# Performance work log

Measured on AMD Instinct MI355X. Metric: run time of the kernel, lower is better.

## Reference

```python
import jax, jax.numpy as jnp
import numpy as np

V, H, T, B = 32000, 1024, 512, 64

def setup_inputs() -> dict:
    key = jax.random.key(0)
    ks = jax.random.split(key, 20)
    tokens = jax.random.randint(ks[0], (T, B), 0, V)
    s_emb = 1.0 / np.sqrt(V)
    s_g = 1.0 / np.sqrt(2 * H)
    d = {
        'tokens': tokens,
        'emb_w': jax.random.uniform(ks[1], (H, V), jnp.float32, -s_emb, s_emb),
        'emb_b': jax.random.uniform(ks[2], (H,), jnp.float32, -s_emb, s_emb),
    }
    i = 3
    for pfx in ('fwd', 'bwd'):
        for g in ('i', 'o', 'f', 'g'):
            d[f'{pfx}_w{g}'] = jax.random.uniform(ks[i], (H, 2 * H), jnp.float32, -s_g, s_g); i += 1
            d[f'{pfx}_b{g}'] = jax.random.uniform(ks[i % 20], (H,), jnp.float32, -s_g, s_g)
    return d

def _run_lstm(xs, wi, bi, wo, bo, wf, bf, wg, bg):
    # xs: [T, B, H]; manual LSTM recurrence via lax.scan
    h0 = jnp.zeros((xs.shape[1], H), xs.dtype)
    c0 = jnp.zeros((xs.shape[1], H), xs.dtype)
    def step(carry, x):
        h, c = carry
        comb = jnp.concatenate([x, h], axis=1)          # [B, 2H]
        ig = jax.nn.sigmoid(comb @ wi.T + bi)
        og = jax.nn.sigmoid(comb @ wo.T + bo)
        fg = jax.nn.sigmoid(comb @ wf.T + bf)
        cg = jnp.tanh(comb @ wg.T + bg)
        c = fg * c + ig * cg
        h = og * jnp.tanh(c)
        return (h, c), (h, c)
    _, (hs, cs) = jax.lax.scan(step, (h0, c0), xs)
    return hs, cs                                       # [T, B, H] each

def reference(tokens, emb_w, emb_b,
              fwd_wi, fwd_bi, fwd_wo, fwd_bo, fwd_wf, fwd_bf, fwd_wg, fwd_bg,
              bwd_wi, bwd_bi, bwd_wo, bwd_bo, bwd_wf, bwd_bf, bwd_wg, bwd_bg):
    # one_hot(tokens) @ emb_w.T + emb_b == emb_w.T[tokens] + emb_b (dropout in eval mode)
    emb = emb_w.T[tokens] + emb_b                        # [T, B, H]
    f_hs, f_cs = _run_lstm(emb, fwd_wi, fwd_bi, fwd_wo, fwd_bo, fwd_wf, fwd_bf, fwd_wg, fwd_bg)
    # backward pass over reversed sequence; outputs kept in reversed-scan order,
    # matching the original's un-realigned list concatenation.
    b_hs, b_cs = _run_lstm(emb[::-1], bwd_wi, bwd_bi, bwd_wo, bwd_bo, bwd_wf, bwd_bf, bwd_wg, bwd_bg)
    hidden_states = jnp.concatenate([f_hs, b_hs], axis=2)   # [T, B, 2H]
    cell_states = jnp.concatenate([f_cs, b_cs], axis=2)     # [T, B, 2H]
    return hidden_states, cell_states
```

## Files before the change

### kernel.cpp

```cpp
#include <hip/hip_runtime.h>
#include <cstdint>
#include <cstddef>

#define V_SZ 32000
#define H_SZ 1024
#define T_SZ 512
#define B_SZ 64

typedef short short8 __attribute__((ext_vector_type(8)));
typedef float f32x4 __attribute__((ext_vector_type(4)));
typedef unsigned long long u64;

__device__ __forceinline__ short f2bf(float f) {
  union { float f; unsigned u; } v; v.f = f;
  unsigned r = (v.u + 0x7fffu + ((v.u >> 16) & 1u)) >> 16;
  return (short)r;
}

__device__ __forceinline__ unsigned cvtpk(float a, float b) {
  unsigned r;
  asm("v_cvt_pk_bf16_f32 %0, %1, %2" : "=v"(r) : "v"(a), "v"(b));
  return r;
}

__device__ __forceinline__ void cs8(u64* p, u64 v) {
  __hip_atomic_store(p, v, __ATOMIC_RELAXED, __HIP_MEMORY_SCOPE_AGENT);
}

__device__ __forceinline__ float fsig(float x) {
  return __builtin_amdgcn_rcpf(1.f + __builtin_amdgcn_exp2f(x * -1.44269504f));
}
__device__ __forceinline__ float ftanh(float x) {
  return 1.f - 2.f * __builtin_amdgcn_rcpf(1.f + __builtin_amdgcn_exp2f(x * 2.88539008f));
}

__global__ __launch_bounds__(256) void k_embT(const float* __restrict__ emb_w,
                                              const float* __restrict__ emb_b,
                                              short* __restrict__ embT) {
  __shared__ float tile[64][65];
  const int v0 = blockIdx.x * 64, h0 = blockIdx.y * 64;
  const int c = threadIdx.x & 63, rg = threadIdx.x >> 6;
#pragma unroll
  for (int p = 0; p < 16; ++p) {
    int r = rg * 16 + p;
    tile[r][c] = emb_w[(size_t)(h0 + r) * V_SZ + v0 + c];
  }
  __syncthreads();
  const float bias = emb_b[h0 + c];
#pragma unroll
  for (int p = 0; p < 16; ++p) {
    int vr = rg * 16 + p;
    embT[(size_t)(v0 + vr) * H_SZ + h0 + c] = f2bf(tile[c][vr] + bias);
  }
}

__global__ __launch_bounds__(256) void k_cast(const float* __restrict__ s,
                                              short* __restrict__ d, int n) {
  for (int i = blockIdx.x * 256 + threadIdx.x; i < n; i += gridDim.x * 256)
    d[i] = f2bf(s[i]);
}

__global__ __launch_bounds__(256) void k_copy(const float* __restrict__ s,
                                              float* __restrict__ d, int n) {
  for (int i = blockIdx.x * 256 + threadIdx.x; i < n; i += gridDim.x * 256)
    d[i] = s[i];
}

__global__ __launch_bounds__(512, 2) void k_persist(
    const int* __restrict__ tokens, const short* __restrict__ embT,
    const short* __restrict__ Wbf, const float* __restrict__ biasws,
    short* __restrict__ hbf, unsigned* __restrict__ bar,
    float* __restrict__ out) {
  __shared__ float P_lds[8][32][68];

  const int tid = threadIdx.x;
  const int lane = tid & 63, w = tid >> 6;
  const int l15 = lane & 15, l4 = lane >> 4;
  const int d = (int)(blockIdx.x >> 7);
  const int bflat = (int)(blockIdx.x & 127);
  const int bg = bflat >> 6;
  const int cg = bflat & 63;
  const int n0 = cg << 4;
  const int r0 = bg * 32 + l15, r1 = r0 + 16;
  const int kw = w * 32 + l4 * 8;

  short8 Bf[8][4];
#pragma unroll
  for (int jj = 0; jj < 8; ++jj) {
    int slab = w + jj * 8;
#pragma unroll
    for (int nt = 0; nt < 4; ++nt) {
      int row64 = nt * 16 + l15;
      size_t grow = (size_t)((d * 4 + (row64 >> 4)) * 1024 + n0 + (row64 & 15));
      Bf[jj][nt] = *(const short8*)(Wbf + grow * 2048 + slab * 32 + l4 * 8);
    }
  }

  const int b32 = tid >> 4, c16 = tid & 15;
  const int gcol = n0 + c16, gbrow = bg * 32 + b32;
  float brg[4];
#pragma unroll
  for (int g4 = 0; g4 < 4; ++g4) brg[g4] = biasws[d * 4096 + g4 * 1024 + gcol];
  float c_reg = 0.f;

  unsigned* const grpf = bar + (d * 2 + bg) * 512;
  unsigned* const fpub = grpf + cg * 8 + w;
  unsigned* const fpoll =
      grpf + ((lane >> 4) * 16 + 2 * w + ((lane >> 3) & 1)) * 8 + (lane & 7);

  const f32x4 fzero = {0.f, 0.f, 0.f, 0.f};
  f32x4 acc[2][4];

  auto X_PHASE = [&](int s) {
    const int td = d ? (T_SZ - 1 - s) : s;
    const short* xb0 = embT + (size_t)tokens[td * B_SZ + r0] * 1024 + kw;
    const short* xb1 = embT + (size_t)tokens[td * B_SZ + r1] * 1024 + kw;
    short8 xf[2][4];
#pragma unroll
    for (int jj = 0; jj < 4; ++jj) {
      xf[0][jj] = *(const short8*)(xb0 + jj * 256);
      xf[1][jj] = *(const short8*)(xb1 + jj * 256);
    }
#pragma unroll
    for (int ms = 0; ms < 2; ++ms)
#pragma unroll
      for (int nt = 0; nt < 4; ++nt) acc[ms][nt] = fzero;
#pragma unroll
    for (int jj = 0; jj < 4; ++jj)
#pragma unroll
      for (int ms = 0; ms < 2; ++ms)
#pragma unroll
        for (int nt = 0; nt < 4; ++nt)
          acc[ms][nt] = __builtin_amdgcn_mfma_f32_16x16x32_bf16(
              xf[ms][jj], Bf[jj][nt], acc[ms][nt], 0, 0, 0);
  };

  X_PHASE(0);

  for (int t = 0; t < T_SZ; ++t) {
    if (t > 0) {
      const unsigned tgt = (unsigned)t;
      while (true) {
        unsigned v = __hip_atomic_load(fpoll, __ATOMIC_RELAXED,
                                       __HIP_MEMORY_SCOPE_AGENT);
        if (__all(v >= tgt)) break;
        __builtin_amdgcn_s_sleep(1);
      }
      const short* hsrc = hbf + ((t & 1) * 2 + d) * 65536;
      const short* hb0 = hsrc + r0 * 1024 + kw;
      const short* hb1 = hsrc + r1 * 1024 + kw;
      short8 hf[2][4];
      asm volatile(
          "global_load_dwordx4 %0, %8, off sc0 sc1\n\t"
          "global_load_dwordx4 %1, %8, off offset:512 sc0 sc1\n\t"
          "global_load_dwordx4 %2, %8, off offset:1024 sc0 sc1\n\t"
          "global_load_dwordx4 %3, %8, off offset:1536 sc0 sc1\n\t"
          "global_load_dwordx4 %4, %9, off sc0 sc1\n\t"
          "global_load_dwordx4 %5, %9, off offset:512 sc0 sc1\n\t"
          "global_load_dwordx4 %6, %9, off offset:1024 sc0 sc1\n\t"
          "global_load_dwordx4 %7, %9, off offset:1536 sc0 sc1\n\t"
          "s_waitcnt vmcnt(0)"
          : "=&v"(hf[0][0]), "=&v"(hf[0][1]), "=&v"(hf[0][2]), "=&v"(hf[0][3]),
            "=&v"(hf[1][0]), "=&v"(hf[1][1]), "=&v"(hf[1][2]), "=&v"(hf[1][3])
          : "v"(hb0), "v"(hb1)
          : "memory");
#pragma unroll
      for (int q = 0; q < 4; ++q)
#pragma unroll
        for (int ms = 0; ms < 2; ++ms)
#pragma unroll
          for (int nt = 0; nt < 4; ++nt)
            acc[ms][nt] = __builtin_amdgcn_mfma_f32_16x16x32_bf16(
                hf[ms][q], Bf[4 + q][nt], acc[ms][nt], 0, 0, 0);
    }

#pragma unroll
    for (int ms = 0; ms < 2; ++ms)
#pragma unroll
      for (int nt = 0; nt < 4; ++nt)
#pragma unroll
        for (int i = 0; i < 4; ++i)
          P_lds[w][ms * 16 + l4 * 4 + i][nt * 16 + l15] = acc[ms][nt][i];
    __syncthreads();

    float pr[4];
#pragma unroll
    for (int g4 = 0; g4 < 4; ++g4) {
      float s = brg[g4];
#pragma unroll
      for (int q = 0; q < 8; ++q) s += P_lds[q][b32][g4 * 16 + c16];
      pr[g4] = s;
    }
    float ig = fsig(pr[0]);
    float og = fsig(pr[1]);
    float fg = fsig(pr[2]);
    float cg4 = ftanh(pr[3]);
    c_reg = fg * c_reg + ig * cg4;
    float hnew = og * ftanh(c_reg);

    if (t < T_SZ - 1) {
      short* hdst = hbf + (((t + 1) & 1) * 2 + d) * 65536;
      float nb = __shfl_down(hnew, 1);
      unsigned ulo = cvtpk(hnew, nb);
      unsigned uhi = __shfl_down(ulo, 2);
      if ((lane & 3) == 0) {
        u64 pk = ((u64)uhi << 32) | (u64)ulo;
        cs8((u64*)(hdst + (size_t)gbrow * 1024 + n0 + (lane & 15)), pk);
      }
      asm volatile("s_waitcnt vmcnt(0)" ::: "memory");
      if (lane == 0)
        __hip_atomic_store(fpub, (unsigned)(t + 1), __ATOMIC_RELAXED,
                           __HIP_MEMORY_SCOPE_AGENT);
    }

    size_t o = (size_t)(t * B_SZ + gbrow) * 2048 + (size_t)d * 1024 + gcol;
    out[o] = hnew;
    out[o + 67108864] = c_reg;

    __syncthreads();
    if (t < T_SZ - 1) X_PHASE(t + 1);
  }
}

extern "C" void kernel_launch(void* const* d_in, const int* in_sizes, int n_in,
                              void* d_out, int out_size, void* d_ws, size_t ws_size,
                              hipStream_t stream) {
  (void)in_sizes; (void)n_in; (void)out_size; (void)ws_size;
  const int* tokens  = (const int*)d_in[0];
  const float* emb_w = (const float*)d_in[1];
  const float* emb_b = (const float*)d_in[2];

  char* ws = (char*)d_ws;
  short* embT   = (short*)(ws);
  short* Wbf    = (short*)(ws + 65536000);
  float* biasws = (float*)(ws + 99090432);
  short* hbf    = (short*)(ws + 99123200);
  unsigned* bar = (unsigned*)(ws + 99647488);

  (void)hipMemsetAsync(ws + 99647488, 0, 8192, stream);

  k_embT<<<dim3(500, 16), 256, 0, stream>>>(emb_w, emb_b, embT);

  for (int d = 0; d < 2; ++d)
    for (int g = 0; g < 4; ++g) {
      const float* wsrc = (const float*)d_in[3 + d * 8 + g * 2];
      const float* bsrc = (const float*)d_in[4 + d * 8 + g * 2];
      k_cast<<<1024, 256, 0, stream>>>(wsrc, Wbf + (size_t)(d * 4 + g) * 1024 * 2048,
                                       1024 * 2048);
      k_copy<<<4, 256, 0, stream>>>(bsrc, biasws + (d * 4 + g) * 1024, 1024);
    }

  float* outp = (float*)d_out;
  void* kargs[] = {(void*)&tokens, (void*)&embT, (void*)&Wbf, (void*)&biasws,
                   (void*)&hbf, (void*)&bar, (void*)&outp};
  (void)hipLaunchCooperativeKernel((const void*)k_persist, dim3(256), dim3(512), kargs,
                                   0, stream);
}
```

Measured before the change: 3.244 ms.

## Write each step's hidden state to its own buffer and drop the per-step barrier

Adds a path that gives every timestep its own bf16 hidden-state slot (hseq), so reads can use plain cached loads instead of sc0/sc1 coherent loads, since each address is written only once. The LDS partial buffer is double-buffered by step parity, which lets the trailing __syncthreads per step be removed. Hidden-state stores are widened to 16-byte stores from fewer lanes. The cached path runs only when the workspace is large enough (about 128MB extra), and it relies on stale-cache avoidance because addresses are never reused.

```diff
diff --git a/kernel.cpp b/kernel.cpp
--- a/kernel.cpp
+++ b/kernel.cpp
@@ -21,10 +21,6 @@
   unsigned r;
   asm("v_cvt_pk_bf16_f32 %0, %1, %2" : "=v"(r) : "v"(a), "v"(b));
   return r;
-}
-
-__device__ __forceinline__ void cs8(u64* p, u64 v) {
-  __hip_atomic_store(p, v, __ATOMIC_RELAXED, __HIP_MEMORY_SCOPE_AGENT);
 }
 
 __device__ __forceinline__ float fsig(float x) {
@@ -66,12 +62,13 @@
     d[i] = s[i];
 }
 
+template <bool CACHED>
 __global__ __launch_bounds__(512, 2) void k_persist(
     const int* __restrict__ tokens, const short* __restrict__ embT,
     const short* __restrict__ Wbf, const float* __restrict__ biasws,
-    short* __restrict__ hbf, unsigned* __restrict__ bar,
-    float* __restrict__ out) {
-  __shared__ float P_lds[8][32][68];
+    short* __restrict__ hbf, short* __restrict__ hseq,
+    unsigned* __restrict__ bar, float* __restrict__ out) {
+  __shared__ float P_lds[2][8][32][68];
 
   const int tid = threadIdx.x;
   const int lane = tid & 63, w = tid >> 6;
@@ -84,6 +81,8 @@
   const int r0 = bg * 32 + l15, r1 = r0 + 16;
   const int kw = w * 32 + l4 * 8;
 
+  __threadfence();
+
   short8 Bf[8][4];
 #pragma unroll
   for (int jj = 0; jj < 8; ++jj) {
@@ -146,24 +145,35 @@
         if (__all(v >= tgt)) break;
         __builtin_amdgcn_s_sleep(1);
       }
-      const short* hsrc = hbf + ((t & 1) * 2 + d) * 65536;
-      const short* hb0 = hsrc + r0 * 1024 + kw;
-      const short* hb1 = hsrc + r1 * 1024 + kw;
       short8 hf[2][4];
-      asm volatile(
-          "global_load_dwordx4 %0, %8, off sc0 sc1\n\t"
-          "global_load_dwordx4 %1, %8, off offset:512 sc0 sc1\n\t"
-          "global_load_dwordx4 %2, %8, off offset:1024 sc0 sc1\n\t"
-          "global_load_dwordx4 %3, %8, off offset:1536 sc0 sc1\n\t"
-          "global_load_dwordx4 %4, %9, off sc0 sc1\n\t"
-          "global_load_dwordx4 %5, %9, off offset:512 sc0 sc1\n\t"
-          "global_load_dwordx4 %6, %9, off offset:1024 sc0 sc1\n\t"
-          "global_load_dwordx4 %7, %9, off offset:1536 sc0 sc1\n\t"
-          "s_waitcnt vmcnt(0)"
-          : "=&v"(hf[0][0]), "=&v"(hf[0][1]), "=&v"(hf[0][2]), "=&v"(hf[0][3]),
-            "=&v"(hf[1][0]), "=&v"(hf[1][1]), "=&v"(hf[1][2]), "=&v"(hf[1][3])
-          : "v"(hb0), "v"(hb1)
-          : "memory");
+      if constexpr (CACHED) {
+        const short* hsrc = hseq + ((size_t)t * 2 + d) * 65536;
+        const short* hb0 = hsrc + r0 * 1024 + kw;
+        const short* hb1 = hsrc + r1 * 1024 + kw;
+#pragma unroll
+        for (int q = 0; q < 4; ++q) {
+          hf[0][q] = *(const short8*)(hb0 + q * 256);
+          hf[1][q] = *(const short8*)(hb1 + q * 256);
+        }
+      } else {
+        const short* hsrc = hbf + ((t & 1) * 2 + d) * 65536;
+        const short* hb0 = hsrc + r0 * 1024 + kw;
+        const short* hb1 = hsrc + r1 * 1024 + kw;
+        asm volatile(
+            "global_load_dwordx4 %0, %8, off sc0 sc1\n\t"
+            "global_load_dwordx4 %1, %8, off offset:512 sc0 sc1\n\t"
+            "global_load_dwordx4 %2, %8, off offset:1024 sc0 sc1\n\t"
+            "global_load_dwordx4 %3, %8, off offset:1536 sc0 sc1\n\t"
+            "global_load_dwordx4 %4, %9, off sc0 sc1\n\t"
+            "global_load_dwordx4 %5, %9, off offset:512 sc0 sc1\n\t"
+            "global_load_dwordx4 %6, %9, off offset:1024 sc0 sc1\n\t"
+            "global_load_dwordx4 %7, %9, off offset:1536 sc0 sc1\n\t"
+            "s_waitcnt vmcnt(0)"
+            : "=&v"(hf[0][0]), "=&v"(hf[0][1]), "=&v"(hf[0][2]), "=&v"(hf[0][3]),
+              "=&v"(hf[1][0]), "=&v"(hf[1][1]), "=&v"(hf[1][2]), "=&v"(hf[1][3])
+            : "v"(hb0), "v"(hb1)
+            : "memory");
+      }
 #pragma unroll
       for (int q = 0; q < 4; ++q)
 #pragma unroll
@@ -180,7 +190,7 @@
       for (int nt = 0; nt < 4; ++nt)
 #pragma unroll
         for (int i = 0; i < 4; ++i)
-          P_lds[w][ms * 16 + l4 * 4 + i][nt * 16 + l15] = acc[ms][nt][i];
+          P_lds[t & 1][w][ms * 16 + l4 * 4 + i][nt * 16 + l15] = acc[ms][nt][i];
     __syncthreads();
 
     float pr[4];
@@ -188,7 +198,7 @@
     for (int g4 = 0; g4 < 4; ++g4) {
       float s = brg[g4];
 #pragma unroll
-      for (int q = 0; q < 8; ++q) s += P_lds[q][b32][g4 * 16 + c16];
+      for (int q = 0; q < 8; ++q) s += P_lds[t & 1][q][b32][g4 * 16 + c16];
       pr[g4] = s;
     }
     float ig = fsig(pr[0]);
@@ -199,13 +209,19 @@
     float hnew = og * ftanh(c_reg);
 
     if (t < T_SZ - 1) {
-      short* hdst = hbf + (((t + 1) & 1) * 2 + d) * 65536;
-      float nb = __shfl_down(hnew, 1);
-      unsigned ulo = cvtpk(hnew, nb);
+      short* hdst = CACHED ? hseq + ((size_t)(t + 1) * 2 + d) * 65536
+                           : hbf + (((t + 1) & 1) * 2 + d) * 65536;
+      float s1 = __shfl_down(hnew, 1);
+      unsigned ulo = cvtpk(hnew, s1);
       unsigned uhi = __shfl_down(ulo, 2);
-      if ((lane & 3) == 0) {
-        u64 pk = ((u64)uhi << 32) | (u64)ulo;
-        cs8((u64*)(hdst + (size_t)gbrow * 1024 + n0 + (lane & 15)), pk);
+      u64 pk = ((u64)uhi << 32) | (u64)ulo;
+      u64 pk4 = __shfl_down(pk, 4);
+      if ((lane & 7) == 0) {
+        union { u64 q[2]; short8 s; } v16;
+        v16.q[0] = pk; v16.q[1] = pk4;
+        short* p = hdst + (size_t)gbrow * 1024 + n0 + (lane & 15);
+        asm volatile("global_store_dwordx4 %0, %1, off sc0 sc1"
+                     :: "v"(p), "v"(v16.s) : "memory");
       }
       asm volatile("s_waitcnt vmcnt(0)" ::: "memory");
       if (lane == 0)
@@ -217,7 +233,6 @@
     out[o] = hnew;
     out[o + 67108864] = c_reg;
 
-    __syncthreads();
     if (t < T_SZ - 1) X_PHASE(t + 1);
   }
 }
@@ -225,7 +240,7 @@
 extern "C" void kernel_launch(void* const* d_in, const int* in_sizes, int n_in,
                               void* d_out, int out_size, void* d_ws, size_t ws_size,
                               hipStream_t stream) {
-  (void)in_sizes; (void)n_in; (void)out_size; (void)ws_size;
+  (void)in_sizes; (void)n_in; (void)out_size;
   const int* tokens  = (const int*)d_in[0];
   const float* emb_w = (const float*)d_in[1];
   const float* emb_b = (const float*)d_in[2];
@@ -236,8 +251,10 @@
   float* biasws = (float*)(ws + 99090432);
   short* hbf    = (short*)(ws + 99123200);
   unsigned* bar = (unsigned*)(ws + 99647488);
-
-  (void)hipMemsetAsync(ws + 99647488, 0, 8192, stream);
+  short* hseq   = (short*)(ws + 99655680);
+  const bool use_cached = ws_size >= (size_t)(99655680 + 134217728);
+
+  (void)hipMemsetAsync(ws + 99123200, 0, 524288 + 8192, stream);
 
   k_embT<<<dim3(500, 16), 256, 0, stream>>>(emb_w, emb_b, embT);
 
@@ -252,7 +269,11 @@
 
   float* outp = (float*)d_out;
   void* kargs[] = {(void*)&tokens, (void*)&embT, (void*)&Wbf, (void*)&biasws,
-                   (void*)&hbf, (void*)&bar, (void*)&outp};
-  (void)hipLaunchCooperativeKernel((const void*)k_persist, dim3(256), dim3(512), kargs,
-                                   0, stream);
-}
+                   (void*)&hbf, (void*)&hseq, (void*)&bar, (void*)&outp};
+  if (use_cached)
+    (void)hipLaunchCooperativeKernel((const void*)k_persist<true>, dim3(256),
+                                     dim3(512), kargs, 0, stream);
+  else
+    (void)hipLaunchCooperativeKernel((const void*)k_persist<false>, dim3(256),
+                                     dim3(512), kargs, 0, stream);
+}
```

Measured after the change: 3.235 ms. About the same (-0.3%).

## Split h-dependency wait into halves, double-buffer LDS partials, widen h stores

Applied to the files above, without the earlier changes.

The persistent LSTM kernel now waits only for the first 32 producer flags before loading and multiplying the first half of the recurrent K slice, then waits for all flags for the second half. This overlaps part of the MFMA work with the grid-wide wait. The partial-sum LDS buffer is double-buffered by timestep parity so the trailing __syncthreads can be dropped. The h publish now uses 16-byte stores from every eighth lane instead of 8-byte atomic stores. The block-to-(direction, batch group, column) mapping is also interleaved, which changes which producers are polled first. All of this relies on the poll-lane ordering matching the new block mapping.

```diff
diff --git a/kernel.cpp b/kernel.cpp
--- a/kernel.cpp
+++ b/kernel.cpp
@@ -21,10 +21,6 @@
   unsigned r;
   asm("v_cvt_pk_bf16_f32 %0, %1, %2" : "=v"(r) : "v"(a), "v"(b));
   return r;
-}
-
-__device__ __forceinline__ void cs8(u64* p, u64 v) {
-  __hip_atomic_store(p, v, __ATOMIC_RELAXED, __HIP_MEMORY_SCOPE_AGENT);
 }
 
 __device__ __forceinline__ float fsig(float x) {
@@ -71,15 +67,16 @@
     const short* __restrict__ Wbf, const float* __restrict__ biasws,
     short* __restrict__ hbf, unsigned* __restrict__ bar,
     float* __restrict__ out) {
-  __shared__ float P_lds[8][32][68];
+  __shared__ float P_lds[2][8][32][68];
 
   const int tid = threadIdx.x;
   const int lane = tid & 63, w = tid >> 6;
   const int l15 = lane & 15, l4 = lane >> 4;
-  const int d = (int)(blockIdx.x >> 7);
-  const int bflat = (int)(blockIdx.x & 127);
-  const int bg = bflat >> 6;
-  const int cg = bflat & 63;
+  const int bid = (int)blockIdx.x;
+  const int m4 = bid & 3;
+  const int d = m4 >> 1;
+  const int bg = m4 & 1;
+  const int cg = bid >> 2;
   const int n0 = cg << 4;
   const int r0 = bg * 32 + l15, r1 = r0 + 16;
   const int kw = w * 32 + l4 * 8;
@@ -140,38 +137,60 @@
   for (int t = 0; t < T_SZ; ++t) {
     if (t > 0) {
       const unsigned tgt = (unsigned)t;
+      const short* hsrc = hbf + ((t & 1) * 2 + d) * 65536;
+      const short* hb0 = hsrc + r0 * 1024 + kw;
+      const short* hb1 = hsrc + r1 * 1024 + kw;
+
+      while (true) {
+        unsigned v = __hip_atomic_load(fpoll, __ATOMIC_RELAXED,
+                                       __HIP_MEMORY_SCOPE_AGENT);
+        u64 rdy = __ballot(v >= tgt);
+        if ((rdy & 0xFFFFFFFFull) == 0xFFFFFFFFull) break;
+        __builtin_amdgcn_s_sleep(1);
+      }
+      short8 hf0[2][2];
+      asm volatile(
+          "global_load_dwordx4 %0, %4, off sc0 sc1\n\t"
+          "global_load_dwordx4 %1, %4, off offset:512 sc0 sc1\n\t"
+          "global_load_dwordx4 %2, %5, off sc0 sc1\n\t"
+          "global_load_dwordx4 %3, %5, off offset:512 sc0 sc1\n\t"
+          "s_waitcnt vmcnt(0)"
+          : "=&v"(hf0[0][0]), "=&v"(hf0[0][1]), "=&v"(hf0[1][0]), "=&v"(hf0[1][1])
+          : "v"(hb0), "v"(hb1)
+          : "memory");
+#pragma unroll
+      for (int q = 0; q < 2; ++q)
+#pragma unroll
+        for (int ms = 0; ms < 2; ++ms)
+#pragma unroll
+          for (int nt = 0; nt < 4; ++nt)
+            acc[ms][nt] = __builtin_amdgcn_mfma_f32_16x16x32_bf16(
+                hf0[ms][q], Bf[4 + q][nt], acc[ms][nt], 0, 0, 0);
+
       while (true) {
         unsigned v = __hip_atomic_load(fpoll, __ATOMIC_RELAXED,
                                        __HIP_MEMORY_SCOPE_AGENT);
         if (__all(v >= tgt)) break;
         __builtin_amdgcn_s_sleep(1);
       }
-      const short* hsrc = hbf + ((t & 1) * 2 + d) * 65536;
-      const short* hb0 = hsrc + r0 * 1024 + kw;
-      const short* hb1 = hsrc + r1 * 1024 + kw;
-      short8 hf[2][4];
+      short8 hf1[2][2];
       asm volatile(
-          "global_load_dwordx4 %0, %8, off sc0 sc1\n\t"
-          "global_load_dwordx4 %1, %8, off offset:512 sc0 sc1\n\t"
-          "global_load_dwordx4 %2, %8, off offset:1024 sc0 sc1\n\t"
-          "global_load_dwordx4 %3, %8, off offset:1536 sc0 sc1\n\t"
-          "global_load_dwordx4 %4, %9, off sc0 sc1\n\t"
-          "global_load_dwordx4 %5, %9, off offset:512 sc0 sc1\n\t"
-          "global_load_dwordx4 %6, %9, off offset:1024 sc0 sc1\n\t"
-          "global_load_dwordx4 %7, %9, off offset:1536 sc0 sc1\n\t"
+          "global_load_dwordx4 %0, %4, off offset:1024 sc0 sc1\n\t"
+          "global_load_dwordx4 %1, %4, off offset:1536 sc0 sc1\n\t"
+          "global_load_dwordx4 %2, %5, off offset:1024 sc0 sc1\n\t"
+          "global_load_dwordx4 %3, %5, off offset:1536 sc0 sc1\n\t"
           "s_waitcnt vmcnt(0)"
-          : "=&v"(hf[0][0]), "=&v"(hf[0][1]), "=&v"(hf[0][2]), "=&v"(hf[0][3]),
-            "=&v"(hf[1][0]), "=&v"(hf[1][1]), "=&v"(hf[1][2]), "=&v"(hf[1][3])
+          : "=&v"(hf1[0][0]), "=&v"(hf1[0][1]), "=&v"(hf1[1][0]), "=&v"(hf1[1][1])
           : "v"(hb0), "v"(hb1)
           : "memory");
 #pragma unroll
-      for (int q = 0; q < 4; ++q)
+      for (int q = 0; q < 2; ++q)
 #pragma unroll
         for (int ms = 0; ms < 2; ++ms)
 #pragma unroll
           for (int nt = 0; nt < 4; ++nt)
             acc[ms][nt] = __builtin_amdgcn_mfma_f32_16x16x32_bf16(
-                hf[ms][q], Bf[4 + q][nt], acc[ms][nt], 0, 0, 0);
+                hf1[ms][q], Bf[6 + q][nt], acc[ms][nt], 0, 0, 0);
     }
 
 #pragma unroll
@@ -180,7 +199,7 @@
       for (int nt = 0; nt < 4; ++nt)
 #pragma unroll
         for (int i = 0; i < 4; ++i)
-          P_lds[w][ms * 16 + l4 * 4 + i][nt * 16 + l15] = acc[ms][nt][i];
+          P_lds[t & 1][w][ms * 16 + l4 * 4 + i][nt * 16 + l15] = acc[ms][nt][i];
     __syncthreads();
 
     float pr[4];
@@ -188,7 +207,7 @@
     for (int g4 = 0; g4 < 4; ++g4) {
       float s = brg[g4];
 #pragma unroll
-      for (int q = 0; q < 8; ++q) s += P_lds[q][b32][g4 * 16 + c16];
+      for (int q = 0; q < 8; ++q) s += P_lds[t & 1][q][b32][g4 * 16 + c16];
       pr[g4] = s;
     }
     float ig = fsig(pr[0]);
@@ -200,12 +219,17 @@
 
     if (t < T_SZ - 1) {
       short* hdst = hbf + (((t + 1) & 1) * 2 + d) * 65536;
-      float nb = __shfl_down(hnew, 1);
-      unsigned ulo = cvtpk(hnew, nb);
+      float s1 = __shfl_down(hnew, 1);
+      unsigned ulo = cvtpk(hnew, s1);
       unsigned uhi = __shfl_down(ulo, 2);
-      if ((lane & 3) == 0) {
-        u64 pk = ((u64)uhi << 32) | (u64)ulo;
-        cs8((u64*)(hdst + (size_t)gbrow * 1024 + n0 + (lane & 15)), pk);
+      u64 pk = ((u64)uhi << 32) | (u64)ulo;
+      u64 pk4 = __shfl_down(pk, 4);
+      if ((lane & 7) == 0) {
+        union { u64 q[2]; short8 s; } v16;
+        v16.q[0] = pk; v16.q[1] = pk4;
+        short* p = hdst + (size_t)gbrow * 1024 + n0 + (lane & 15);
+        asm volatile("global_store_dwordx4 %0, %1, off sc0 sc1"
+                     :: "v"(p), "v"(v16.s) : "memory");
       }
       asm volatile("s_waitcnt vmcnt(0)" ::: "memory");
       if (lane == 0)
@@ -217,7 +241,6 @@
     out[o] = hnew;
     out[o + 67108864] = c_reg;
 
-    __syncthreads();
     if (t < T_SZ - 1) X_PHASE(t + 1);
   }
 }
@@ -253,6 +276,6 @@
   float* outp = (float*)d_out;
   void* kargs[] = {(void*)&tokens, (void*)&embT, (void*)&Wbf, (void*)&biasws,
                    (void*)&hbf, (void*)&bar, (void*)&outp};
-  (void)hipLaunchCooperativeKernel((const void*)k_persist, dim3(256), dim3(512), kargs,
-                                   0, stream);
-}
+  (void)hipLaunchCooperativeKernel((const void*)k_persist, dim3(256), dim3(512),
+                                   kargs, 0, stream);
+}
```

New measurement: 3.117 ms. -3.9%, faster.
